# Kernel optimization log

Measured on AMD Instinct MI355X. Metric: run time of the kernel, lower is better.

The kernel has to match this reference:

```python
import jax, jax.numpy as jnp
import numpy as np

B, S, D, H, E, K, V, FF, P = 1, 2048, 1024, 16, 8, 2, 32000, 4096, 4096
HD = D // H
EPS = 1e-5


def setup_inputs() -> dict:
    key = jax.random.key(0)
    ks = iter(jax.random.split(key, 64))
    w = lambda shape: jax.random.normal(next(ks), shape, jnp.float32) * 0.02
    d = {}
    d['input_ids'] = jax.random.randint(next(ks), (B, S), 0, V)
    d['embed_w'] = w((V, D))
    d['pos_w'] = w((P, D))
    for i in (0, 1):
        d[f'b{i}_ln1_g'] = jnp.ones(D); d[f'b{i}_ln1_b'] = jnp.zeros(D)
        d[f'b{i}_in_w'] = w((3 * D, D)); d[f'b{i}_in_b'] = jnp.zeros(3 * D)
        d[f'b{i}_out_w'] = w((D, D)); d[f'b{i}_out_b'] = jnp.zeros(D)
        d[f'b{i}_ln2_g'] = jnp.ones(D); d[f'b{i}_ln2_b'] = jnp.zeros(D)
    d['b0_ffn_w1'] = w((FF, D)); d['b0_ffn_b1'] = jnp.zeros(FF)
    d['b0_ffn_w2'] = w((D, FF)); d['b0_ffn_b2'] = jnp.zeros(D)
    d['b1_gate_w'] = w((E, D)); d['b1_gate_b'] = jnp.zeros(E)
    d['b1_moe_w1'] = w((E, FF, D)); d['b1_moe_b1'] = jnp.zeros((E, FF))
    d['b1_moe_w2'] = w((E, D, FF)); d['b1_moe_b2'] = jnp.zeros((E, D))
    d['norm_g'] = jnp.ones(D); d['norm_b'] = jnp.zeros(D)
    d['head_w'] = w((V, D))
    return d


def _ln(x, g, b):
    m = jnp.mean(x, -1, keepdims=True)
    v = jnp.mean(jnp.square(x - m), -1, keepdims=True)
    return (x - m) * jax.lax.rsqrt(v + EPS) * g + b


def _mha(x, in_w, in_b, out_w, out_b):
    # torch nn.MultiheadAttention (batch_first, eval mode -> no dropout)
    qkv = x @ in_w.T + in_b  # [B,S,3D]
    q, k, v = jnp.split(qkv, 3, axis=-1)
    q = q.reshape(B, S, H, HD); k = k.reshape(B, S, H, HD); v = v.reshape(B, S, H, HD)
    scores = jnp.einsum('bqhd,bkhd->bhqk', q, k) / jnp.sqrt(jnp.float32(HD))
    attn = jax.nn.softmax(scores, axis=-1)
    o = jnp.einsum('bhqk,bkhd->bqhd', attn, v).reshape(B, S, D)
    return o @ out_w.T + out_b


def _moe(h, gate_w, gate_b, w1, b1, w2, b2):
    scores = h @ gate_w.T + gate_b                       # [B,S,E]
    top_s, top_i = jax.lax.top_k(scores, K)              # [B,S,K]
    weights = jax.nn.softmax(top_s, axis=-1)             # softmax over top-k
    onehot = jax.nn.one_hot(top_i, E, dtype=h.dtype)     # [B,S,K,E]
    combine = jnp.sum(onehot * weights[..., None], axis=-2)  # [B,S,E]
    hid = jax.nn.gelu(jnp.einsum('bsd,efd->bsef', h, w1) + b1, approximate=False)
    eo = jnp.einsum('bsef,edf->bsed', hid, w2) + b2      # [B,S,E,D]
    return jnp.einsum('bsed,bse->bsd', eo, combine)


def reference(input_ids, embed_w, pos_w,
              b0_ln1_g, b0_ln1_b, b0_in_w, b0_in_b, b0_out_w, b0_out_b, b0_ln2_g, b0_ln2_b,
              b0_ffn_w1, b0_ffn_b1, b0_ffn_w2, b0_ffn_b2,
              b1_ln1_g, b1_ln1_b, b1_in_w, b1_in_b, b1_out_w, b1_out_b, b1_ln2_g, b1_ln2_b,
              b1_gate_w, b1_gate_b, b1_moe_w1, b1_moe_b1, b1_moe_w2, b1_moe_b2,
              norm_g, norm_b, head_w):
    pos = jnp.arange(S)[None, :]
    x = jnp.take(embed_w, input_ids, axis=0) + jnp.take(pos_w, pos, axis=0)
    # block 0: dense FFN
    x = x + _mha(_ln(x, b0_ln1_g, b0_ln1_b), b0_in_w, b0_in_b, b0_out_w, b0_out_b)
    h = _ln(x, b0_ln2_g, b0_ln2_b)
    ffn = jax.nn.gelu(h @ b0_ffn_w1.T + b0_ffn_b1, approximate=False) @ b0_ffn_w2.T + b0_ffn_b2
    x = x + ffn  # integration layer assumed residual add
    # block 1: MoE
    x = x + _mha(_ln(x, b1_ln1_g, b1_ln1_b), b1_in_w, b1_in_b, b1_out_w, b1_out_b)
    h = _ln(x, b1_ln2_g, b1_ln2_b)
    x = x + _moe(h, b1_gate_w, b1_gate_b, b1_moe_w1, b1_moe_b1, b1_moe_w2, b1_moe_b2)
    x = _ln(x, norm_g, norm_b)
    return x @ head_w.T
```

## Files before the change

kernel.cpp:

```cpp
#include <hip/hip_runtime.h>
#include <hip/hip_bf16.h>
#include <math.h>

typedef unsigned short ushort_t;
typedef __attribute__((ext_vector_type(8))) __bf16 bf16x8;
typedef __attribute__((ext_vector_type(4))) float f32x4;
typedef __attribute__((ext_vector_type(8))) short s8v;
typedef __attribute__((ext_vector_type(4))) short s4v;

#define SQ 2048
#define DM 1024
#define NH 16
#define HDIM 64
#define FFD 4096
#define NVOC 32000

__device__ inline float b2f(unsigned short u) {
  union { unsigned int i; float f; } x; x.i = ((unsigned int)u) << 16; return x.f;
}
__device__ inline unsigned short f2b(float f) {
  __hip_bfloat16 h = __float2bfloat16(f);
  return *reinterpret_cast<unsigned short*>(&h);
}
__device__ inline void split2(float x, ushort_t& h, ushort_t& l) {
  h = f2b(x);
  l = f2b(x - b2f(h));
}
__device__ inline float geluf(float v) {
  return 0.5f * v * (1.0f + erff(v * 0.70710678118654752f));
}
__device__ __forceinline__ void gld16(const void* g, void* l) {
  __builtin_amdgcn_global_load_lds(
      (const __attribute__((address_space(1))) void*)g,
      (__attribute__((address_space(3))) void*)l, 16, 0, 0);
}
#define MFMA __builtin_amdgcn_mfma_f32_16x16x32_bf16

template<int EPI, int NT, int KS>
__device__ __forceinline__ void gemmsp_body(
    const ushort_t* __restrict__ AH, const ushort_t* __restrict__ AL,
    int lda, long long bA,
    const ushort_t* __restrict__ BH, const ushort_t* __restrict__ BL,
    int ldb, long long bB,
    float* __restrict__ C, ushort_t* __restrict__ CH, ushort_t* __restrict__ CL,
    int ldc, long long bC, long long pC,
    int M, int N, int K, const float* __restrict__ bias, float alpha,
    ushort_t* __restrict__ TH, ushort_t* __restrict__ TL)
{
  int z = blockIdx.z, h = z / KS, kc = z % KS;
  const ushort_t* AHp = AH + (long long)h * bA + (long long)kc * K;
  const ushort_t* ALp = AL + (long long)h * bA + (long long)kc * K;
  const ushort_t* BHp = BH + (long long)h * bB + (long long)kc * K;
  const ushort_t* BLp = BL + (long long)h * bB + (long long)kc * K;
  int m0 = blockIdx.x * 128, n0 = blockIdx.y * NT;
  const int NF = NT / 32;

  __shared__ __align__(16) ushort_t sAH[2][128 * 32], sAL[2][128 * 32];
  __shared__ __align__(16) ushort_t sBH[2][NT * 32],  sBL[2][NT * 32];

  int tid = threadIdx.x, lane = tid & 63, wave = tid >> 6;
  int wr = (wave >> 1) * 64, wc = (wave & 1) * (NT >> 1);
  int l15 = lane & 15, l4 = lane >> 4;

  f32x4 acc[4][NF];
#pragma unroll
  for (int m = 0; m < 4; ++m)
#pragma unroll
    for (int n = 0; n < NF; ++n) acc[m][n] = (f32x4){0.f, 0.f, 0.f, 0.f};

  auto stageG = [&](int buf, int k0) {
#pragma unroll
    for (int i = 0; i < 2; ++i) {
      int fi = i * 2048 + tid * 8;
      int r = fi >> 5, chk = (fi >> 3) & 3;
      int scol = ((chk ^ ((r >> 1) & 3)) << 3);
      int ra = m0 + r; if (ra > M - 1) ra = M - 1;
      long long go = (long long)ra * lda + k0 + scol;
      gld16(AHp + go, &sAH[buf][fi]);
      gld16(ALp + go, &sAL[buf][fi]);
    }
#pragma unroll
    for (int i = 0; i < NT / 64; ++i) {
      int fi = i * 2048 + tid * 8;
      int r = fi >> 5, chk = (fi >> 3) & 3;
      int scol = ((chk ^ ((r >> 1) & 3)) << 3);
      int rb = n0 + r; if (rb > N - 1) rb = N - 1;
      long long go = (long long)rb * ldb + k0 + scol;
      gld16(BHp + go, &sBH[buf][fi]);
      gld16(BLp + go, &sBL[buf][fi]);
    }
  };

  int nIt = K >> 5;
  stageG(0, 0);
  for (int it = 0; it < nIt; ++it) {
    int cur = it & 1;
    __syncthreads();
    if (it + 1 < nIt) stageG(cur ^ 1, (it + 1) << 5);
    bf16x8 ah[4], al[4], bh[NF], bl[NF];
#pragma unroll
    for (int m = 0; m < 4; ++m) {
      int r = wr + m * 16 + l15;
      int o = r * 32 + ((l4 ^ ((r >> 1) & 3)) << 3);
      ah[m] = *(const bf16x8*)&sAH[cur][o];
      al[m] = *(const bf16x8*)&sAL[cur][o];
    }
#pragma unroll
    for (int n = 0; n < NF; ++n) {
      int r = wc + n * 16 + l15;
      int o = r * 32 + ((l4 ^ ((r >> 1) & 3)) << 3);
      bh[n] = *(const bf16x8*)&sBH[cur][o];
      bl[n] = *(const bf16x8*)&sBL[cur][o];
    }
#pragma unroll
    for (int m = 0; m < 4; ++m)
#pragma unroll
      for (int n = 0; n < NF; ++n) {
        acc[m][n] = MFMA(ah[m], bh[n], acc[m][n], 0, 0, 0);
        acc[m][n] = MFMA(al[m], bh[n], acc[m][n], 0, 0, 0);
        acc[m][n] = MFMA(ah[m], bl[n], acc[m][n], 0, 0, 0);
      }
  }

  if (EPI == 5 && n0 >= 2 * DM) {
#pragma unroll
    for (int m = 0; m < 4; ++m) {
      int rbase = m0 + wr + m * 16 + l4 * 4;
#pragma unroll
      for (int n = 0; n < NF; ++n) {
        int c = n0 + wc + n * 16 + l15;
        int d = c - 2 * DM;
        float bv = bias[c];
        s4v hv, lv;
#pragma unroll
        for (int q = 0; q < 4; ++q) {
          ushort_t hh, ll; split2(acc[m][n][q] + bv, hh, ll);
          hv[q] = (short)hh; lv[q] = (short)ll;
        }
        *(s4v*)&TH[(long long)d * SQ + rbase] = hv;
        *(s4v*)&TL[(long long)d * SQ + rbase] = lv;
      }
    }
    return;
  }

#pragma unroll
  for (int m = 0; m < 4; ++m) {
#pragma unroll
    for (int n = 0; n < NF; ++n) {
      int c = n0 + wc + n * 16 + l15;
      if (c >= N) continue;
      float bv = (EPI == 4 || EPI == 5) ? bias[c] : 0.f;
#pragma unroll
      for (int q = 0; q < 4; ++q) {
        int rr = m0 + wr + m * 16 + l4 * 4 + q;
        if (rr >= M) continue;
        float v = acc[m][n][q];
        if (EPI == 5) {
          ushort_t hh, ll; split2(v + bv, hh, ll);
          long long o = (long long)rr * ldc + c; CH[o] = hh; CL[o] = ll;
        } else if (EPI == 2) {
          C[(long long)kc * pC + (long long)rr * ldc + (long long)h * bC + c] = v;
        } else if (EPI == 4) {
          ushort_t hh, ll; split2(geluf(v + bv), hh, ll);
          long long o = (long long)rr * ldc + c; CH[o] = hh; CL[o] = ll;
        }
      }
    }
  }
}

#define SP_ARGS const ushort_t* AH, const ushort_t* AL, int lda, long long bA, \
    const ushort_t* BH, const ushort_t* BL, int ldb, long long bB, \
    float* C, ushort_t* CH, ushort_t* CL, int ldc, long long bC, long long pC, \
    int M, int N, int K, const float* bias, float alpha, \
    ushort_t* TH, ushort_t* TL
#define SP_PASS AH, AL, lda, bA, BH, BL, ldb, bB, C, CH, CL, ldc, bC, pC, M, N, K, bias, alpha, TH, TL

__global__ __launch_bounds__(256) void k_qkv (SP_ARGS) { gemmsp_body<5,128,1>(SP_PASS); }
__global__ __launch_bounds__(256) void k_outp(SP_ARGS) { gemmsp_body<2, 64,4>(SP_PASS); }
__global__ __launch_bounds__(256) void k_ffn1(SP_ARGS) { gemmsp_body<4,128,1>(SP_PASS); }
__global__ __launch_bounds__(256) void k_ffn2(SP_ARGS) { gemmsp_body<2, 64,2>(SP_PASS); }

__global__ __launch_bounds__(256)
void k_attn(const ushort_t* __restrict__ qkvH, const ushort_t* __restrict__ qkvL,
            const ushort_t* __restrict__ VtH, const ushort_t* __restrict__ VtL,
            ushort_t* __restrict__ aH, ushort_t* __restrict__ aL)
{
  int f = blockIdx.x + blockIdx.y * gridDim.x;
  int logical = (f & 7) * 64 + (f >> 3);
  int q0 = (logical & 31) * 64;
  int h  = logical >> 5;

  __shared__ __align__(16) ushort_t sKH[2][4096], sKL[2][4096];
  __shared__ __align__(16) ushort_t sVH[2][4096], sVL[2][4096];
  __shared__ __align__(16) ushort_t sPH[4096], sPL[4096];

  int tid = threadIdx.x, lane = tid & 63, wave = tid >> 6;
  int l15 = lane & 15, l4 = lane >> 4;

  bf16x8 qh[2], ql[2];
  {
    long long base = (long long)(q0 + wave * 16 + l15) * (3 * DM) + h * 64 + l4 * 8;
    qh[0] = *(const bf16x8*)(qkvH + base);
    qh[1] = *(const bf16x8*)(qkvH + base + 32);
    ql[0] = *(const bf16x8*)(qkvL + base);
    ql[1] = *(const bf16x8*)(qkvL + base + 32);
  }

  auto stageKV = [&](int buf, int kt) {
#pragma unroll
    for (int i = 0; i < 2; ++i) {
      int idx = i * 2048 + tid * 8;
      int row = idx >> 6, chk = (idx >> 3) & 7;
      int scol = ((chk ^ (row & 7)) << 3);
      long long gk = (long long)(kt * 64 + row) * (3 * DM) + DM + h * 64 + scol;
      long long gv = (long long)(h * 64 + row) * SQ + kt * 64 + scol;
      gld16(qkvH + gk, &sKH[buf][idx]);
      gld16(qkvL + gk, &sKL[buf][idx]);
      gld16(VtH + gv, &sVH[buf][idx]);
      gld16(VtL + gv, &sVL[buf][idx]);
    }
  };

  float mrow[4], lrow[4];
  f32x4 Oacc[4];
#pragma unroll
  for (int r = 0; r < 4; ++r) { mrow[r] = -1e30f; lrow[r] = 0.f; }
#pragma unroll
  for (int n = 0; n < 4; ++n) Oacc[n] = (f32x4){0.f, 0.f, 0.f, 0.f};

  const int NT = SQ / 64;
  stageKV(0, 0);
  for (int kt = 0; kt < NT; ++kt) {
    int cur = kt & 1;
    __syncthreads();
    if (kt + 1 < NT) stageKV(cur ^ 1, kt + 1);

    f32x4 S[4];
#pragma unroll
    for (int n = 0; n < 4; ++n) S[n] = (f32x4){0.f, 0.f, 0.f, 0.f};
#pragma unroll
    for (int kk = 0; kk < 64; kk += 32) {
      int kkI = kk >> 5;
      bf16x8 qhf = qh[kkI], qlf = ql[kkI];
#pragma unroll
      for (int n = 0; n < 4; ++n) {
        int br = n * 16 + l15;
        int bo = br * 64 + ((((kk >> 3) + l4) ^ (br & 7)) << 3);
        bf16x8 kh = *(const bf16x8*)&sKH[cur][bo];
        bf16x8 kl = *(const bf16x8*)&sKL[cur][bo];
        S[n] = MFMA(qhf, kh, S[n], 0, 0, 0);
        S[n] = MFMA(qlf, kh, S[n], 0, 0, 0);
        S[n] = MFMA(qhf, kl, S[n], 0, 0, 0);
      }
    }
    float tm[4], ts[4];
#pragma unroll
    for (int r = 0; r < 4; ++r) {
#pragma unroll
      for (int n = 0; n < 4; ++n) S[n][r] *= 0.125f;
      tm[r] = fmaxf(fmaxf(S[0][r], S[1][r]), fmaxf(S[2][r], S[3][r]));
    }
#pragma unroll
    for (int mk = 1; mk <= 8; mk <<= 1)
#pragma unroll
      for (int r = 0; r < 4; ++r) tm[r] = fmaxf(tm[r], __shfl_xor(tm[r], mk));
#pragma unroll
    for (int r = 0; r < 4; ++r) {
      float mn = fmaxf(mrow[r], tm[r]);
      float corr = __expf(mrow[r] - mn);
      mrow[r] = mn;
      float s = 0.f;
#pragma unroll
      for (int n = 0; n < 4; ++n) { S[n][r] = __expf(S[n][r] - mn); s += S[n][r]; }
      ts[r] = s;
      lrow[r] *= corr;
#pragma unroll
      for (int n = 0; n < 4; ++n) Oacc[n][r] *= corr;
    }
#pragma unroll
    for (int mk = 1; mk <= 8; mk <<= 1)
#pragma unroll
      for (int r = 0; r < 4; ++r) ts[r] += __shfl_xor(ts[r], mk);
#pragma unroll
    for (int r = 0; r < 4; ++r) lrow[r] += ts[r];

    {
      ushort_t* pH = &sPH[wave * 1024];
      ushort_t* pL = &sPL[wave * 1024];
#pragma unroll
      for (int n = 0; n < 4; ++n)
#pragma unroll
        for (int r = 0; r < 4; ++r) {
          int row = l4 * 4 + r, col = n * 16 + l15;
          int ad = row * 64 + (((col >> 3) ^ (row & 7)) << 3) + (col & 7);
          ushort_t hh, ll; split2(S[n][r], hh, ll);
          pH[ad] = hh; pL[ad] = ll;
        }
    }
    __syncthreads();
#pragma unroll
    for (int kk = 0; kk < 64; kk += 32) {
      int ao = wave * 1024 + l15 * 64 + ((((kk >> 3) + l4) ^ (l15 & 7)) << 3);
      bf16x8 ph = *(const bf16x8*)&sPH[ao];
      bf16x8 pl = *(const bf16x8*)&sPL[ao];
#pragma unroll
      for (int n = 0; n < 4; ++n) {
        int br = n * 16 + l15;
        int bo = br * 64 + ((((kk >> 3) + l4) ^ (br & 7)) << 3);
        bf16x8 vh = *(const bf16x8*)&sVH[cur][bo];
        bf16x8 vl = *(const bf16x8*)&sVL[cur][bo];
        Oacc[n] = MFMA(ph, vh, Oacc[n], 0, 0, 0);
        Oacc[n] = MFMA(pl, vh, Oacc[n], 0, 0, 0);
        Oacc[n] = MFMA(ph, vl, Oacc[n], 0, 0, 0);
      }
    }
  }

#pragma unroll
  for (int n = 0; n < 4; ++n)
#pragma unroll
    for (int r = 0; r < 4; ++r) {
      int q = q0 + wave * 16 + l4 * 4 + r;
      int d = h * 64 + n * 16 + l15;
      float val = Oacc[n][r] / lrow[r];
      ushort_t hh, ll; split2(val, hh, ll);
      long long o = (long long)q * DM + d;
      aH[o] = hh; aL[o] = ll;
    }
}

template<int EPI, int SWAP, int KS>
__device__ __forceinline__ void gemm16s_body(
    const ushort_t* __restrict__ A, int lda, long long bA,
    const ushort_t* __restrict__ Bp0, int ldb, long long bB,
    void* __restrict__ Cv, int ldc, long long bC, long long pC,
    int M, int N, int K, const float* __restrict__ bias, int bBias,
    const int* __restrict__ offs)
{
  int bz = blockIdx.z;
  int z = bz / KS, kc = bz % KS;
  int Kc = K / KS;
  const ushort_t* Ap = A + (long long)z * bA + (long long)kc * Kc;
  const ushort_t* Bp = Bp0 + (long long)z * bB + (long long)kc * Kc;
  int rowStart = 0, Meff = M;
  if (offs) { rowStart = offs[z]; Meff = offs[z + 1] - rowStart; }
  int m0 = (SWAP ? blockIdx.y : blockIdx.x) * 128;
  if (m0 >= Meff) return;
  int n0 = (SWAP ? blockIdx.x : blockIdx.y) * 128;

  __shared__ __align__(16) char smem[32768];

  int tid = threadIdx.x, lane = tid & 63, wave = tid >> 6;
  int wr = (wave >> 1) * 64, wc = (wave & 1) * 64;
  int l15 = lane & 15, l4 = lane >> 4;

  f32x4 acc[4][4];
#pragma unroll
  for (int m = 0; m < 4; ++m)
#pragma unroll
    for (int n = 0; n < 4; ++n) acc[m][n] = (f32x4){0.f, 0.f, 0.f, 0.f};

  auto stageG = [&](int buf, int k0) {
    ushort_t* dA = (ushort_t*)(smem + buf * 8192);
    ushort_t* dB = (ushort_t*)(smem + 16384 + buf * 8192);
#pragma unroll
    for (int i = 0; i < 2; ++i) {
      int idx = i * 2048 + tid * 8;
      int row = idx >> 5, chk = (idx >> 3) & 3;
      int scol = ((chk ^ ((row >> 1) & 3)) << 3);
      int ra = m0 + row; if (ra > Meff - 1) ra = Meff - 1;
      gld16(Ap + (long long)(rowStart + ra) * lda + k0 + scol, &dA[idx]);
    }
#pragma unroll
    for (int i = 0; i < 2; ++i) {
      int idx = i * 2048 + tid * 8;
      int row = idx >> 5, chk = (idx >> 3) & 3;
      int scol = ((chk ^ ((row >> 1) & 3)) << 3);
      int rb = n0 + row; if (rb > N - 1) rb = N - 1;
      gld16(Bp + (long long)rb * ldb + k0 + scol, &dB[idx]);
    }
  };

  int nIt = Kc >> 5;
  stageG(0, 0);
  for (int it = 0; it < nIt; ++it) {
    int cur = it & 1;
    __syncthreads();
    if (it + 1 < nIt) stageG(cur ^ 1, (it + 1) << 5);
    ushort_t* As = (ushort_t*)(smem + cur * 8192);
    ushort_t* Bs = (ushort_t*)(smem + 16384 + cur * 8192);
    bf16x8 af[4], bfr[4];
#pragma unroll
    for (int m = 0; m < 4; ++m) {
      int r = wr + m * 16 + l15;
      af[m] = *(const bf16x8*)&As[r * 32 + ((l4 ^ ((r >> 1) & 3)) << 3)];
    }
#pragma unroll
    for (int n = 0; n < 4; ++n) {
      int r = wc + n * 16 + l15;
      bfr[n] = *(const bf16x8*)&Bs[r * 32 + ((l4 ^ ((r >> 1) & 3)) << 3)];
    }
#pragma unroll
    for (int m = 0; m < 4; ++m)
#pragma unroll
      for (int n = 0; n < 4; ++n)
        acc[m][n] = MFMA(af[m], bfr[n], acc[m][n], 0, 0, 0);
  }
  __syncthreads();

  if (EPI == 7) {
    float* fE = (float*)smem;
#pragma unroll
    for (int h2 = 0; h2 < 2; ++h2) {
      if ((wave >> 1) == h2) {
#pragma unroll
        for (int m = 0; m < 4; ++m)
#pragma unroll
          for (int n = 0; n < 4; ++n)
#pragma unroll
            for (int q = 0; q < 4; ++q)
              fE[(m * 16 + l4 * 4 + q) * 128 + wc + n * 16 + l15] = acc[m][n][q];
      }
      __syncthreads();
#pragma unroll
      for (int i = 0; i < 8; ++i) {
        int lin = tid + i * 256;
        int row = lin >> 5, c4 = (lin & 31) << 2;
        int gr = m0 + h2 * 64 + row;
        if (gr < Meff) {
          f32x4 v4 = *(const f32x4*)&fE[row * 128 + c4];
          long long crow = rowStart + gr;
          float* dst = (float*)Cv + (long long)kc * pC + crow * ldc + n0 + c4;
          *(f32x4*)dst = v4;
        }
      }
      __syncthreads();
    }
    return;
  }

#pragma unroll
  for (int m = 0; m < 4; ++m) {
#pragma unroll
    for (int n = 0; n < 4; ++n) {
      int c = n0 + wc + n * 16 + l15;
      if (c >= N) continue;
      float bv = (EPI == 2) ? bias[(long long)z * bBias + c] : 0.f;
#pragma unroll
      for (int q = 0; q < 4; ++q) {
        int rr = m0 + wr + m * 16 + l4 * 4 + q;
        if (rr >= Meff) continue;
        float v = acc[m][n][q];
        long long crow = rowStart + rr;
        if (EPI == 2)
          ((ushort_t*)Cv)[crow * ldc + (long long)z * bC + c] = f2b(geluf(v + bv));
      }
    }
  }
}

template<int BSRC>
__device__ __forceinline__ void gemm16w_body(
    const ushort_t* __restrict__ A, int lda,
    const void* __restrict__ Bv, int ldb,
    float* __restrict__ Cv, int ldc,
    int M, int N, int K)
{
  int bx = blockIdx.x, by = blockIdx.y;
  {
    int flat = bx + by * gridDim.x;
    int cpx = (gridDim.x * gridDim.y) >> 3;
    int s = (flat & 7) * cpx + (flat >> 3);
    bx = s % gridDim.x; by = s / gridDim.x;
  }
  int m0 = bx * 256;
  int n0 = by * 128;

  __shared__ __align__(16) char smem[49152];
  const ushort_t* Bp = (BSRC == 1) ? (const ushort_t*)Bv : nullptr;
  const float* Bf = (BSRC == 0) ? (const float*)Bv : nullptr;

  int tid = threadIdx.x, lane = tid & 63, wave = tid >> 6;
  int wr = (wave >> 1) * 128, wc = (wave & 1) * 64;
  int l15 = lane & 15, l4 = lane >> 4;

  f32x4 acc[8][4];
#pragma unroll
  for (int m = 0; m < 8; ++m)
#pragma unroll
    for (int n = 0; n < 4; ++n) acc[m][n] = (f32x4){0.f, 0.f, 0.f, 0.f};

  auto stageG = [&](int buf, int k0) {
    ushort_t* dA = (ushort_t*)(smem + buf * 16384);
    ushort_t* dB = (ushort_t*)(smem + 32768 + buf * 8192);
#pragma unroll
    for (int i = 0; i < 4; ++i) {
      int idx = i * 2048 + tid * 8;
      int row = idx >> 5, chk = (idx >> 3) & 3;
      int scol = ((chk ^ ((row >> 1) & 3)) << 3);
      int ra = m0 + row; if (ra > M - 1) ra = M - 1;
      gld16(A + (long long)ra * lda + k0 + scol, &dA[idx]);
    }
    if (BSRC == 1) {
#pragma unroll
      for (int i = 0; i < 2; ++i) {
        int idx = i * 2048 + tid * 8;
        int row = idx >> 5, chk = (idx >> 3) & 3;
        int scol = ((chk ^ ((row >> 1) & 3)) << 3);
        int rb = n0 + row; if (rb > N - 1) rb = N - 1;
        gld16(Bp + (long long)rb * ldb + k0 + scol, &dB[idx]);
      }
    } else {
#pragma unroll
      for (int i = 0; i < 4; ++i) {
        int g = tid + i * 256;
        int r = g >> 3, c4 = (g & 7) * 4;
        int rb = n0 + r; if (rb > N - 1) rb = N - 1;
        float4 fv = *(const float4*)(Bf + (long long)rb * ldb + k0 + c4);
        s4v o; o[0] = (short)f2b(fv.x); o[1] = (short)f2b(fv.y);
        o[2] = (short)f2b(fv.z); o[3] = (short)f2b(fv.w);
        int dst = r * 32 + ((((c4 >> 3) ^ ((r >> 1) & 3))) << 3) + (c4 & 7);
        *(s4v*)&dB[dst] = o;
      }
    }
  };

  int nIt = K >> 5;
  stageG(0, 0);
  for (int it = 0; it < nIt; ++it) {
    int cur = it & 1;
    __syncthreads();
    if (it + 1 < nIt) stageG(cur ^ 1, (it + 1) << 5);
    ushort_t* As = (ushort_t*)(smem + cur * 16384);
    ushort_t* Bs = (ushort_t*)(smem + 32768 + cur * 8192);
    bf16x8 af[8], bfr[4];
#pragma unroll
    for (int m = 0; m < 8; ++m) {
      int r = wr + m * 16 + l15;
      af[m] = *(const bf16x8*)&As[r * 32 + ((l4 ^ ((r >> 1) & 3)) << 3)];
    }
#pragma unroll
    for (int n = 0; n < 4; ++n) {
      int r = wc + n * 16 + l15;
      bfr[n] = *(const bf16x8*)&Bs[r * 32 + ((l4 ^ ((r >> 1) & 3)) << 3)];
    }
#pragma unroll
    for (int m = 0; m < 8; ++m)
#pragma unroll
      for (int n = 0; n < 4; ++n)
        acc[m][n] = MFMA(af[m], bfr[n], acc[m][n], 0, 0, 0);
  }
  __syncthreads();

  float* fE = (float*)smem;
#pragma unroll
  for (int h2 = 0; h2 < 4; ++h2) {
    if ((wave >> 1) == (h2 >> 1)) {
#pragma unroll
      for (int mm = 0; mm < 4; ++mm) {
        int m = (h2 & 1) * 4 + mm;
#pragma unroll
        for (int n = 0; n < 4; ++n)
#pragma unroll
          for (int q = 0; q < 4; ++q)
            fE[(mm * 16 + l4 * 4 + q) * 128 + wc + n * 16 + l15] = acc[m][n][q];
      }
    }
    __syncthreads();
#pragma unroll
    for (int i = 0; i < 8; ++i) {
      int lin = tid + i * 256;
      int row = lin >> 5, c4 = (lin & 31) << 2;
      int gr = m0 + h2 * 64 + row;
      if (gr < M) {
        f32x4 v4 = *(const f32x4*)&fE[row * 128 + c4];
        float* dst = Cv + (long long)gr * ldc + n0 + c4;
        __builtin_nontemporal_store(v4, (f32x4*)dst);
      }
    }
    __syncthreads();
  }
}

#define G16_ARGS const ushort_t* A, int lda, long long bA, const void* Bv, \
    int ldb, long long bB, void* Cv, int ldc, long long bC, long long pC, \
    int M, int N, int K, const float* bias, int bBias, const int* offs
#define G16S_PASS(EPI,SWAP,KS) gemm16s_body<EPI,SWAP,KS>(A, lda, bA, \
    (const ushort_t*)Bv, ldb, bB, Cv, ldc, bC, pC, M, N, K, bias, bBias, offs)

__global__ __launch_bounds__(256) void k_moe1(G16_ARGS) { G16S_PASS(2,1,1); }
__global__ __launch_bounds__(256) void k_moe2(G16_ARGS) { G16S_PASS(7,1,2); }
__global__ __launch_bounds__(256) void k_head_bf(G16_ARGS) {
  gemm16w_body<1>(A, lda, Bv, ldb, (float*)Cv, ldc, M, N, K);
}
__global__ __launch_bounds__(256) void k_head_f(G16_ARGS) {
  gemm16w_body<0>(A, lda, Bv, ldb, (float*)Cv, ldc, M, N, K);
}

__global__ __launch_bounds__(256)
void cvt_split2(const float* __restrict__ s0, ushort_t* __restrict__ dh0,
                ushort_t* __restrict__ dl0,
                const float* __restrict__ s1, ushort_t* __restrict__ dh1,
                ushort_t* __restrict__ dl1, int n4)
{
  const float* s = blockIdx.y ? s1 : s0;
  ushort_t* dh = blockIdx.y ? dh1 : dh0;
  ushort_t* dl = blockIdx.y ? dl1 : dl0;
  int i = blockIdx.x * blockDim.x + threadIdx.x;
  int stride = gridDim.x * blockDim.x;
  for (; i < n4; i += stride) {
    float4 f = ((const float4*)s)[i];
    s4v h, l; ushort_t hh, ll;
    split2(f.x, hh, ll); h[0] = (short)hh; l[0] = (short)ll;
    split2(f.y, hh, ll); h[1] = (short)hh; l[1] = (short)ll;
    split2(f.z, hh, ll); h[2] = (short)hh; l[2] = (short)ll;
    split2(f.w, hh, ll); h[3] = (short)hh; l[3] = (short)ll;
    ((s4v*)dh)[i] = h; ((s4v*)dl)[i] = l;
  }
}

__global__ __launch_bounds__(256)
void cvt_bf16(const float* __restrict__ s, ushort_t* __restrict__ d, int n4)
{
  int i = blockIdx.x * blockDim.x + threadIdx.x;
  int stride = gridDim.x * blockDim.x;
  for (; i < n4; i += stride) {
    float4 f = ((const float4*)s)[i];
    s4v o; o[0] = (short)f2b(f.x); o[1] = (short)f2b(f.y);
    o[2] = (short)f2b(f.z); o[3] = (short)f2b(f.w);
    ((s4v*)d)[i] = o;
  }
}

__global__ __launch_bounds__(256)
void cvt_bf16_2(const float* __restrict__ s0, ushort_t* __restrict__ d0,
                const float* __restrict__ s1, ushort_t* __restrict__ d1, int n4)
{
  const float* s = blockIdx.y ? s1 : s0;
  ushort_t* d = blockIdx.y ? d1 : d0;
  int i = blockIdx.x * blockDim.x + threadIdx.x;
  int stride = gridDim.x * blockDim.x;
  for (; i < n4; i += stride) {
    float4 f = ((const float4*)s)[i];
    s4v o; o[0] = (short)f2b(f.x); o[1] = (short)f2b(f.y);
    o[2] = (short)f2b(f.z); o[3] = (short)f2b(f.w);
    ((s4v*)d)[i] = o;
  }
}

__global__ __launch_bounds__(256)
void embed_kernel(const int* __restrict__ ids, const float* __restrict__ ew,
                  const float* __restrict__ pw, float* __restrict__ x,
                  int* __restrict__ counts)
{
  int srow = blockIdx.x, tid = threadIdx.x;
  if (srow == 0 && tid < 8) counts[tid] = 0;
  int id = ids[srow];
  const float4 e = *(const float4*)(ew + (long long)id * DM + tid * 4);
  const float4 p = *(const float4*)(pw + (long long)srow * DM + tid * 4);
  float4* xr = (float4*)(x + (long long)srow * DM) + tid;
  *xr = make_float4(e.x + p.x, e.y + p.y, e.z + p.z, e.w + p.w);
}

template<int MODE, int NP>
__global__ __launch_bounds__(256)
void ln_fused(float* __restrict__ x, const float* __restrict__ P, long long pC,
              const float* __restrict__ bias_pre,
              const float* __restrict__ g, const float* __restrict__ b,
              ushort_t* __restrict__ outH, ushort_t* __restrict__ outL)
{
  int row = blockIdx.x, tid = threadIdx.x;
  long long xo = (long long)row * DM + tid * 4;
  float4 v = *(const float4*)(x + xo);
  if (NP > 0) {
    float4 bp = *(const float4*)(bias_pre + tid * 4);
    float sx = bp.x, sy = bp.y, sz = bp.z, sw = bp.w;
#pragma unroll
    for (int p = 0; p < NP; ++p) {
      float4 pv = *(const float4*)(P + (long long)p * pC + xo);
      sx += pv.x; sy += pv.y; sz += pv.z; sw += pv.w;
    }
    v.x += sx; v.y += sy; v.z += sz; v.w += sw;
    *(float4*)(x + xo) = v;
  }
  __shared__ float sm1[4], sm2[4];
  float s = v.x + v.y + v.z + v.w;
  for (int o = 32; o > 0; o >>= 1) s += __shfl_down(s, o);
  if ((tid & 63) == 0) sm1[tid >> 6] = s;
  __syncthreads();
  float mean = (sm1[0] + sm1[1] + sm1[2] + sm1[3]) * (1.0f / DM);
  float d0 = v.x - mean, d1 = v.y - mean, d2 = v.z - mean, d3 = v.w - mean;
  float q = d0 * d0 + d1 * d1 + d2 * d2 + d3 * d3;
  for (int o = 32; o > 0; o >>= 1) q += __shfl_down(q, o);
  if ((tid & 63) == 0) sm2[tid >> 6] = q;
  __syncthreads();
  float var = (sm2[0] + sm2[1] + sm2[2] + sm2[3]) * (1.0f / DM);
  float rstd = rsqrtf(var + 1e-5f);
  float4 gv = ((const float4*)g)[tid];
  float4 bv = ((const float4*)b)[tid];
  float o0 = d0 * rstd * gv.x + bv.x, o1 = d1 * rstd * gv.y + bv.y;
  float o2 = d2 * rstd * gv.z + bv.z, o3 = d3 * rstd * gv.w + bv.w;
  long long base = (long long)row * DM + tid * 4;
  if (MODE == 0) {
    ushort_t hh, ll;
    split2(o0, hh, ll); outH[base + 0] = hh; outL[base + 0] = ll;
    split2(o1, hh, ll); outH[base + 1] = hh; outL[base + 1] = ll;
    split2(o2, hh, ll); outH[base + 2] = hh; outL[base + 2] = ll;
    split2(o3, hh, ll); outH[base + 3] = hh; outL[base + 3] = ll;
  } else {
    outH[base + 0] = f2b(o0); outH[base + 1] = f2b(o1);
    outH[base + 2] = f2b(o2); outH[base + 3] = f2b(o3);
  }
}

__global__ __launch_bounds__(256)
void ln_gate_top2(float* __restrict__ x, const float* __restrict__ P,
                  long long pC, const float* __restrict__ bias_pre,
                  const float* __restrict__ g, const float* __restrict__ b,
                  const float* __restrict__ gw, const float* __restrict__ gb,
                  int* __restrict__ topi, float* __restrict__ topw,
                  int* __restrict__ counts, ushort_t* __restrict__ outH)
{
  int row = blockIdx.x, tid = threadIdx.x;
  long long xo = (long long)row * DM + tid * 4;
  float4 v = *(const float4*)(x + xo);
  {
    float4 bp = *(const float4*)(bias_pre + tid * 4);
    float sx = bp.x, sy = bp.y, sz = bp.z, sw = bp.w;
#pragma unroll
    for (int p = 0; p < 4; ++p) {
      float4 pv = *(const float4*)(P + (long long)p * pC + xo);
      sx += pv.x; sy += pv.y; sz += pv.z; sw += pv.w;
    }
    v.x += sx; v.y += sy; v.z += sz; v.w += sw;
    *(float4*)(x + xo) = v;
  }
  __shared__ float sm1[4], sm2[4];
  __shared__ float se[8][4];
  float s = v.x + v.y + v.z + v.w;
  for (int o = 32; o > 0; o >>= 1) s += __shfl_down(s, o);
  if ((tid & 63) == 0) sm1[tid >> 6] = s;
  __syncthreads();
  float mean = (sm1[0] + sm1[1] + sm1[2] + sm1[3]) * (1.0f / DM);
  float d0 = v.x - mean, d1 = v.y - mean, d2 = v.z - mean, d3 = v.w - mean;
  float q = d0 * d0 + d1 * d1 + d2 * d2 + d3 * d3;
  for (int o = 32; o > 0; o >>= 1) q += __shfl_down(q, o);
  if ((tid & 63) == 0) sm2[tid >> 6] = q;
  __syncthreads();
  float var = (sm2[0] + sm2[1] + sm2[2] + sm2[3]) * (1.0f / DM);
  float rstd = rsqrtf(var + 1e-5f);
  float4 gv = ((const float4*)g)[tid];
  float4 bv = ((const float4*)b)[tid];
  float h0 = d0 * rstd * gv.x + bv.x, h1 = d1 * rstd * gv.y + bv.y;
  float h2 = d2 * rstd * gv.z + bv.z, h3 = d3 * rstd * gv.w + bv.w;
  long long base = (long long)row * DM + tid * 4;
  outH[base + 0] = f2b(h0); outH[base + 1] = f2b(h1);
  outH[base + 2] = f2b(h2); outH[base + 3] = f2b(h3);
#pragma unroll
  for (int e = 0; e < 8; ++e) {
    float4 w = ((const float4*)(gw + (long long)e * DM))[tid];
    float p = h0 * w.x + h1 * w.y + h2 * w.z + h3 * w.w;
    for (int o = 32; o > 0; o >>= 1) p += __shfl_down(p, o);
    if ((tid & 63) == 0) se[e][tid >> 6] = p;
  }
  __syncthreads();
  if (tid == 0) {
    float sc[8];
#pragma unroll
    for (int e = 0; e < 8; ++e)
      sc[e] = se[e][0] + se[e][1] + se[e][2] + se[e][3] + gb[e];
    int i1 = 0; float m1 = sc[0];
    for (int e = 1; e < 8; ++e) if (sc[e] > m1) { m1 = sc[e]; i1 = e; }
    int i2 = -1; float m2 = -1e30f;
    for (int e = 0; e < 8; ++e) if (e != i1 && sc[e] > m2) { m2 = sc[e]; i2 = e; }
    float e2 = __expf(m2 - m1);
    float w1 = 1.f / (1.f + e2);
    topi[row * 2] = i1; topi[row * 2 + 1] = i2;
    topw[row * 2] = w1; topw[row * 2 + 1] = 1.f - w1;
    atomicAdd(&counts[i1], 1);
    atomicAdd(&counts[i2], 1);
  }
}

__global__ void moe_prefix(const int* __restrict__ counts, int* __restrict__ offs,
                           int* __restrict__ cursors)
{
  if (threadIdx.x == 0 && blockIdx.x == 0) {
    int a = 0;
    for (int e = 0; e < 8; ++e) { offs[e] = a; a += counts[e]; cursors[e] = 0; }
    offs[8] = a;
  }
}

__global__ __launch_bounds__(256)
void moe_gather(const ushort_t* __restrict__ hH, const int* __restrict__ topi,
                const float* __restrict__ topw, const int* __restrict__ offs,
                int* __restrict__ cursors, int* __restrict__ tokIdx,
                float* __restrict__ tokW, int* __restrict__ slotOf,
                ushort_t* __restrict__ Xg)
{
  int tok = blockIdx.x, tid = threadIdx.x;
  __shared__ int s0s, s1s;
  if (tid == 0) {
    int e0 = topi[tok * 2], e1 = topi[tok * 2 + 1];
    int s0 = offs[e0] + atomicAdd(&cursors[e0], 1);
    int s1 = offs[e1] + atomicAdd(&cursors[e1], 1);
    tokIdx[s0] = tok; tokW[s0] = topw[tok * 2];
    tokIdx[s1] = tok; tokW[s1] = topw[tok * 2 + 1];
    slotOf[tok * 2] = s0; slotOf[tok * 2 + 1] = s1;
    s0s = s0; s1s = s1;
  }
  __syncthreads();
  s4v v = ((const s4v*)(hH + (long long)tok * DM))[tid];
  ((s4v*)(Xg + (long long)s0s * DM))[tid] = v;
  ((s4v*)(Xg + (long long)s1s * DM))[tid] = v;
}

__global__ __launch_bounds__(256)
void moe_ln_final(const float* __restrict__ x, const float* __restrict__ eo,
                  long long pC, const int* __restrict__ slotOf,
                  const int* __restrict__ topi, const float* __restrict__ topw,
                  const float* __restrict__ b2, const float* __restrict__ g,
                  const float* __restrict__ b, ushort_t* __restrict__ outH)
{
  int tok = blockIdx.x, tid = threadIdx.x;
  int s0 = slotOf[tok * 2], s1 = slotOf[tok * 2 + 1];
  int e0 = topi[tok * 2], e1 = topi[tok * 2 + 1];
  float w0 = topw[tok * 2], w1 = topw[tok * 2 + 1];
  float4 a  = ((const float4*)(eo + (long long)s0 * DM))[tid];
  float4 a2 = ((const float4*)(eo + pC + (long long)s0 * DM))[tid];
  float4 bb1= ((const float4*)(eo + (long long)s1 * DM))[tid];
  float4 bb2= ((const float4*)(eo + pC + (long long)s1 * DM))[tid];
  float4 ba = ((const float4*)(b2 + (long long)e0 * DM))[tid];
  float4 bbb= ((const float4*)(b2 + (long long)e1 * DM))[tid];
  float4 v = ((const float4*)(x + (long long)tok * DM))[tid];
  v.x += w0 * (a.x + a2.x + ba.x) + w1 * (bb1.x + bb2.x + bbb.x);
  v.y += w0 * (a.y + a2.y + ba.y) + w1 * (bb1.y + bb2.y + bbb.y);
  v.z += w0 * (a.z + a2.z + ba.z) + w1 * (bb1.z + bb2.z + bbb.z);
  v.w += w0 * (a.w + a2.w + ba.w) + w1 * (bb1.w + bb2.w + bbb.w);
  __shared__ float sm1[4], sm2[4];
  float s = v.x + v.y + v.z + v.w;
  for (int o = 32; o > 0; o >>= 1) s += __shfl_down(s, o);
  if ((tid & 63) == 0) sm1[tid >> 6] = s;
  __syncthreads();
  float mean = (sm1[0] + sm1[1] + sm1[2] + sm1[3]) * (1.0f / DM);
  float d0 = v.x - mean, d1 = v.y - mean, d2 = v.z - mean, d3 = v.w - mean;
  float q = d0 * d0 + d1 * d1 + d2 * d2 + d3 * d3;
  for (int o = 32; o > 0; o >>= 1) q += __shfl_down(q, o);
  if ((tid & 63) == 0) sm2[tid >> 6] = q;
  __syncthreads();
  float var = (sm2[0] + sm2[1] + sm2[2] + sm2[3]) * (1.0f / DM);
  float rstd = rsqrtf(var + 1e-5f);
  float4 gv = ((const float4*)g)[tid];
  float4 bv = ((const float4*)b)[tid];
  long long base = (long long)tok * DM + tid * 4;
  outH[base + 0] = f2b(d0 * rstd * gv.x + bv.x);
  outH[base + 1] = f2b(d1 * rstd * gv.y + bv.y);
  outH[base + 2] = f2b(d2 * rstd * gv.z + bv.z);
  outH[base + 3] = f2b(d3 * rstd * gv.w + bv.w);
}

extern "C" void kernel_launch(void* const* d_in, const int* in_sizes, int n_in,
                              void* d_out, int out_size, void* d_ws, size_t ws_size,
                              hipStream_t stream)
{
  const int* ids = (const int*)d_in[0];
  const float* embed_w = (const float*)d_in[1];
  const float* pos_w   = (const float*)d_in[2];
  const float* ln1_g[2] = {(const float*)d_in[3],  (const float*)d_in[11]};
  const float* ln1_b[2] = {(const float*)d_in[4],  (const float*)d_in[12]};
  const float* in_w[2]  = {(const float*)d_in[5],  (const float*)d_in[13]};
  const float* in_b[2]  = {(const float*)d_in[6],  (const float*)d_in[14]};
  const float* out_w[2] = {(const float*)d_in[7],  (const float*)d_in[15]};
  const float* out_b[2] = {(const float*)d_in[8],  (const float*)d_in[16]};
  const float* ln2_g[2] = {(const float*)d_in[9],  (const float*)d_in[17]};
  const float* ln2_b[2] = {(const float*)d_in[10], (const float*)d_in[18]};
  const float* ffn_w1 = (const float*)d_in[19];
  const float* ffn_b1 = (const float*)d_in[20];
  const float* ffn_w2 = (const float*)d_in[21];
  const float* ffn_b2 = (const float*)d_in[22];
  const float* gate_w = (const float*)d_in[23];
  const float* gate_b = (const float*)d_in[24];
  const float* moe_w1 = (const float*)d_in[25];
  const float* moe_b1 = (const float*)d_in[26];
  const float* moe_w2 = (const float*)d_in[27];
  const float* moe_b2 = (const float*)d_in[28];
  const float* norm_g = (const float*)d_in[29];
  const float* norm_b = (const float*)d_in[30];
  const float* head_w = (const float*)d_in[31];

  char* ob = (char*)d_out;
  size_t off = 0;
  auto alloc = [&](size_t bytes) {
    char* p = ob + off;
    off = (off + bytes + 255) & ~(size_t)255;
    return p;
  };
  float*    x      = (float*)alloc((size_t)SQ * DM * 4);
  ushort_t* hbufH  = (ushort_t*)alloc((size_t)SQ * DM * 2);
  ushort_t* hbufL  = (ushort_t*)alloc((size_t)SQ * DM * 2);
  ushort_t* qkvH   = (ushort_t*)alloc((size_t)SQ * 3 * DM * 2);
  ushort_t* qkvL   = (ushort_t*)alloc((size_t)SQ * 3 * DM * 2);
  ushort_t* VtH    = (ushort_t*)alloc((size_t)NH * HDIM * SQ * 2);
  ushort_t* VtL    = (ushort_t*)alloc((size_t)NH * HDIM * SQ * 2);
  char*     resv   = (char*)alloc((size_t)32 << 20);
  ushort_t* attnH  = (ushort_t*)alloc((size_t)SQ * DM * 2);
  ushort_t* attnL  = (ushort_t*)alloc((size_t)SQ * DM * 2);
  ushort_t* Xg     = (ushort_t*)alloc((size_t)2 * SQ * DM * 2);
  int*      topi   = (int*)alloc(SQ * 2 * 4);
  float*    topw   = (float*)alloc(SQ * 2 * 4);
  int*      tokIdx = (int*)alloc(2 * SQ * 4);
  float*    tokW   = (float*)alloc(2 * SQ * 4);
  int*      slotOf = (int*)alloc(2 * SQ * 4);
  int*      counts = (int*)alloc(256);
  int*      offsb  = (int*)alloc(256);
  int*      cursors= (int*)alloc(256);
  ushort_t* ffnH   = (ushort_t*)alloc((size_t)SQ * FFD * 2);
  ushort_t* ffnL   = (ushort_t*)alloc((size_t)SQ * FFD * 2);
  float*    eo     = (float*)alloc((size_t)2 * 2 * SQ * DM * 4);
  ushort_t* inwH[2], *inwL[2], *outwH[2], *outwL[2];
  ushort_t* wsplit0 = (ushort_t*)alloc(0);
  inwH[0]  = (ushort_t*)alloc((size_t)3 * DM * DM * 2);
  inwL[0]  = (ushort_t*)alloc((size_t)3 * DM * DM * 2);
  inwH[1]  = (ushort_t*)alloc((size_t)3 * DM * DM * 2);
  inwL[1]  = (ushort_t*)alloc((size_t)3 * DM * DM * 2);
  outwH[0] = (ushort_t*)alloc((size_t)DM * DM * 2);
  outwL[0] = (ushort_t*)alloc((size_t)DM * DM * 2);
  outwH[1] = (ushort_t*)alloc((size_t)DM * DM * 2);
  outwL[1] = (ushort_t*)alloc((size_t)DM * DM * 2);
  ushort_t* f1H = (ushort_t*)alloc((size_t)FFD * DM * 2);
  ushort_t* f1L = (ushort_t*)alloc((size_t)FFD * DM * 2);
  ushort_t* f2H = (ushort_t*)alloc((size_t)DM * FFD * 2);
  ushort_t* f2L = (ushort_t*)alloc((size_t)DM * FFD * 2);
  ushort_t* moe_w1b = wsplit0;
  ushort_t* moe_w2b = qkvH;
  ushort_t* moehid  = ffnH;
  float*    pp      = eo;
  const long long eoPC = (long long)2 * SQ * DM;
  const long long ppPC = (long long)SQ * DM;
  ushort_t* hfin    = (ushort_t*)d_ws;
  bool wsBig = ws_size >= ((size_t)70 << 20);
  ushort_t* head_wb = (ushort_t*)((char*)d_ws + ((size_t)4 << 20));
  (void)resv;

  embed_kernel<<<SQ, 256, 0, stream>>>(ids, embed_w, pos_w, x, counts);
  cvt_split2<<<dim3(512, 2), 256, 0, stream>>>(
      in_w[0], inwH[0], inwL[0], in_w[1], inwH[1], inwL[1], 3 * DM * DM / 4);
  cvt_split2<<<dim3(512, 2), 256, 0, stream>>>(
      out_w[0], outwH[0], outwL[0], out_w[1], outwH[1], outwL[1], DM * DM / 4);
  cvt_split2<<<dim3(512, 2), 256, 0, stream>>>(
      ffn_w1, f1H, f1L, ffn_w2, f2H, f2L, FFD * DM / 4);
  if (wsBig)
    cvt_bf16<<<1024, 256, 0, stream>>>(head_w, head_wb, NVOC * DM / 4);

  ln_fused<0, 0><<<SQ, 256, 0, stream>>>(x, nullptr, 0, nullptr,
                                         ln1_g[0], ln1_b[0], hbufH, hbufL);
  k_qkv<<<dim3(16, 24, 1), 256, 0, stream>>>(
      hbufH, hbufL, DM, 0, inwH[0], inwL[0], DM, 0,
      nullptr, qkvH, qkvL, 3 * DM, 0, 0,
      SQ, 3 * DM, DM, in_b[0], 1.f, VtH, VtL);
  k_attn<<<dim3(SQ / 64, NH), 256, 0, stream>>>(qkvH, qkvL, VtH, VtL,
                                                attnH, attnL);
  k_outp<<<dim3(16, 16, 4), 256, 0, stream>>>(
      attnH, attnL, DM, 0, outwH[0], outwL[0], DM, 0,
      pp, nullptr, nullptr, DM, 0, ppPC,
      SQ, DM, DM / 4, nullptr, 1.f, nullptr, nullptr);
  ln_fused<0, 4><<<SQ, 256, 0, stream>>>(x, pp, ppPC, out_b[0],
                                         ln2_g[0], ln2_b[0], hbufH, hbufL);
  k_ffn1<<<dim3(16, 32, 1), 256, 0, stream>>>(
      hbufH, hbufL, DM, 0, f1H, f1L, DM, 0,
      nullptr, ffnH, ffnL, FFD, 0, 0,
      SQ, FFD, DM, ffn_b1, 1.f, nullptr, nullptr);
  k_ffn2<<<dim3(16, 16, 2), 256, 0, stream>>>(
      ffnH, ffnL, FFD, 0, f2H, f2L, FFD, 0,
      pp, nullptr, nullptr, DM, 0, ppPC,
      SQ, DM, FFD / 2, nullptr, 1.f, nullptr, nullptr);
  ln_fused<0, 2><<<SQ, 256, 0, stream>>>(x, pp, ppPC, ffn_b2,
                                         ln1_g[1], ln1_b[1], hbufH, hbufL);
  k_qkv<<<dim3(16, 24, 1), 256, 0, stream>>>(
      hbufH, hbufL, DM, 0, inwH[1], inwL[1], DM, 0,
      nullptr, qkvH, qkvL, 3 * DM, 0, 0,
      SQ, 3 * DM, DM, in_b[1], 1.f, VtH, VtL);
  k_attn<<<dim3(SQ / 64, NH), 256, 0, stream>>>(qkvH, qkvL, VtH, VtL,
                                                attnH, attnL);
  k_outp<<<dim3(16, 16, 4), 256, 0, stream>>>(
      attnH, attnL, DM, 0, outwH[1], outwL[1], DM, 0,
      pp, nullptr, nullptr, DM, 0, ppPC,
      SQ, DM, DM / 4, nullptr, 1.f, nullptr, nullptr);
  cvt_bf16_2<<<dim3(2048, 2), 256, 0, stream>>>(
      moe_w1, moe_w1b, moe_w2, moe_w2b, 8 * FFD * DM / 4);
  ln_gate_top2<<<SQ, 256, 0, stream>>>(x, pp, ppPC, out_b[1],
                                       ln2_g[1], ln2_b[1], gate_w, gate_b,
                                       topi, topw, counts, hbufH);
  moe_prefix<<<1, 64, 0, stream>>>(counts, offsb, cursors);
  moe_gather<<<SQ, 256, 0, stream>>>(hbufH, topi, topw, offsb, cursors,
                                     tokIdx, tokW, slotOf, Xg);
  k_moe1<<<dim3(32, 16, 8), 256, 0, stream>>>(
      Xg, DM, 0, moe_w1b, DM, (long long)FFD * DM,
      moehid, FFD, 0, 0, SQ, FFD, DM, moe_b1, FFD, offsb);
  k_moe2<<<dim3(8, 16, 16), 256, 0, stream>>>(
      moehid, FFD, 0, moe_w2b, FFD, (long long)DM * FFD,
      eo, DM, 0, eoPC, SQ, DM, FFD, nullptr, 0, offsb);
  moe_ln_final<<<SQ, 256, 0, stream>>>(x, eo, eoPC, slotOf, topi, topw,
                                       moe_b2, norm_g, norm_b, hfin);
  if (wsBig)
    k_head_bf<<<dim3(8, 250, 1), 256, 0, stream>>>(
        hfin, DM, 0, head_wb, DM, 0, d_out, NVOC, 0, 0,
        SQ, NVOC, DM, nullptr, 0, nullptr);
  else
    k_head_f<<<dim3(8, 250, 1), 256, 0, stream>>>(
        hfin, DM, 0, head_w, DM, 0, d_out, NVOC, 0, 0,
        SQ, NVOC, DM, nullptr, 0, nullptr);
}
```

Measured before the change: 1.126 ms.

## Deepen bf16 head GEMM prefetch to two stages with explicit vmcnt waits

The bf16-weight vocab-head GEMM now gets its own body. It issues global-to-LDS loads two k-steps ahead and uses manual s_waitcnt vmcnt counts plus raw s_barrier in place of __syncthreads each iteration. LDS fragments are read into registers before the barrier, so the next stage can overwrite the same buffer while the MFMAs run. The fp32-weight path is split into a separate unchanged function. The aim is to hide global load latency in the large head GEMM, at the cost of fragile hand-tuned wait counts.

```diff
diff --git a/kernel.cpp b/kernel.cpp
--- a/kernel.cpp
+++ b/kernel.cpp
@@ -461,10 +461,9 @@
   }
 }
 
-template<int BSRC>
-__device__ __forceinline__ void gemm16w_body(
+__device__ __forceinline__ void gemm16w8_body(
     const ushort_t* __restrict__ A, int lda,
-    const void* __restrict__ Bv, int ldb,
+    const ushort_t* __restrict__ Bp, int ldb,
     float* __restrict__ Cv, int ldc,
     int M, int N, int K)
 {
@@ -479,8 +478,6 @@
   int n0 = by * 128;
 
   __shared__ __align__(16) char smem[49152];
-  const ushort_t* Bp = (BSRC == 1) ? (const ushort_t*)Bv : nullptr;
-  const float* Bf = (BSRC == 0) ? (const float*)Bv : nullptr;
 
   int tid = threadIdx.x, lane = tid & 63, wave = tid >> 6;
   int wr = (wave >> 1) * 128, wc = (wave & 1) * 64;
@@ -503,27 +500,138 @@
       int ra = m0 + row; if (ra > M - 1) ra = M - 1;
       gld16(A + (long long)ra * lda + k0 + scol, &dA[idx]);
     }
-    if (BSRC == 1) {
-#pragma unroll
-      for (int i = 0; i < 2; ++i) {
-        int idx = i * 2048 + tid * 8;
-        int row = idx >> 5, chk = (idx >> 3) & 3;
-        int scol = ((chk ^ ((row >> 1) & 3)) << 3);
-        int rb = n0 + row; if (rb > N - 1) rb = N - 1;
-        gld16(Bp + (long long)rb * ldb + k0 + scol, &dB[idx]);
+#pragma unroll
+    for (int i = 0; i < 2; ++i) {
+      int idx = i * 2048 + tid * 8;
+      int row = idx >> 5, chk = (idx >> 3) & 3;
+      int scol = ((chk ^ ((row >> 1) & 3)) << 3);
+      int rb = n0 + row; if (rb > N - 1) rb = N - 1;
+      gld16(Bp + (long long)rb * ldb + k0 + scol, &dB[idx]);
+    }
+  };
+
+  int nIt = K >> 5;
+  stageG(0, 0);
+  stageG(1, 32);
+  asm volatile("s_waitcnt vmcnt(6)" ::: "memory");
+  __builtin_amdgcn_s_barrier();
+  __builtin_amdgcn_sched_barrier(0);
+
+  for (int it = 0; it < nIt; ++it) {
+    int cur = it & 1;
+    ushort_t* As = (ushort_t*)(smem + cur * 16384);
+    ushort_t* Bs = (ushort_t*)(smem + 32768 + cur * 8192);
+    bf16x8 af[8], bfr[4];
+#pragma unroll
+    for (int m = 0; m < 8; ++m) {
+      int r = wr + m * 16 + l15;
+      af[m] = *(const bf16x8*)&As[r * 32 + ((l4 ^ ((r >> 1) & 3)) << 3)];
+    }
+#pragma unroll
+    for (int n = 0; n < 4; ++n) {
+      int r = wc + n * 16 + l15;
+      bfr[n] = *(const bf16x8*)&Bs[r * 32 + ((l4 ^ ((r >> 1) & 3)) << 3)];
+    }
+    asm volatile("s_waitcnt lgkmcnt(0)" ::: "memory");
+    __builtin_amdgcn_sched_barrier(0);
+    __builtin_amdgcn_s_barrier();
+    __builtin_amdgcn_sched_barrier(0);
+    if (it + 2 < nIt) stageG(cur, (it + 2) << 5);
+#pragma unroll
+    for (int m = 0; m < 8; ++m)
+#pragma unroll
+      for (int n = 0; n < 4; ++n)
+        acc[m][n] = MFMA(af[m], bfr[n], acc[m][n], 0, 0, 0);
+    if (it + 1 < nIt) {
+      if (it + 2 < nIt)
+        asm volatile("s_waitcnt vmcnt(6)" ::: "memory");
+      else
+        asm volatile("s_waitcnt vmcnt(0)" ::: "memory");
+      __builtin_amdgcn_s_barrier();
+      __builtin_amdgcn_sched_barrier(0);
+    }
+  }
+  __syncthreads();
+
+  float* fE = (float*)smem;
+#pragma unroll
+  for (int h2 = 0; h2 < 4; ++h2) {
+    if ((wave >> 1) == (h2 >> 1)) {
+#pragma unroll
+      for (int mm = 0; mm < 4; ++mm) {
+        int m = (h2 & 1) * 4 + mm;
+#pragma unroll
+        for (int n = 0; n < 4; ++n)
+#pragma unroll
+          for (int q = 0; q < 4; ++q)
+            fE[(mm * 16 + l4 * 4 + q) * 128 + wc + n * 16 + l15] = acc[m][n][q];
       }
-    } else {
-#pragma unroll
-      for (int i = 0; i < 4; ++i) {
-        int g = tid + i * 256;
-        int r = g >> 3, c4 = (g & 7) * 4;
-        int rb = n0 + r; if (rb > N - 1) rb = N - 1;
-        float4 fv = *(const float4*)(Bf + (long long)rb * ldb + k0 + c4);
-        s4v o; o[0] = (short)f2b(fv.x); o[1] = (short)f2b(fv.y);
-        o[2] = (short)f2b(fv.z); o[3] = (short)f2b(fv.w);
-        int dst = r * 32 + ((((c4 >> 3) ^ ((r >> 1) & 3))) << 3) + (c4 & 7);
-        *(s4v*)&dB[dst] = o;
+    }
+    __syncthreads();
+#pragma unroll
+    for (int i = 0; i < 8; ++i) {
+      int lin = tid + i * 256;
+      int row = lin >> 5, c4 = (lin & 31) << 2;
+      int gr = m0 + h2 * 64 + row;
+      if (gr < M) {
+        f32x4 v4 = *(const f32x4*)&fE[row * 128 + c4];
+        float* dst = Cv + (long long)gr * ldc + n0 + c4;
+        __builtin_nontemporal_store(v4, (f32x4*)dst);
       }
+    }
+    __syncthreads();
+  }
+}
+
+__device__ __forceinline__ void gemm16w_body_f(
+    const ushort_t* __restrict__ A, int lda,
+    const float* __restrict__ Bf, int ldb,
+    float* __restrict__ Cv, int ldc,
+    int M, int N, int K)
+{
+  int bx = blockIdx.x, by = blockIdx.y;
+  {
+    int flat = bx + by * gridDim.x;
+    int cpx = (gridDim.x * gridDim.y) >> 3;
+    int s = (flat & 7) * cpx + (flat >> 3);
+    bx = s % gridDim.x; by = s / gridDim.x;
+  }
+  int m0 = bx * 256;
+  int n0 = by * 128;
+
+  __shared__ __align__(16) char smem[49152];
+
+  int tid = threadIdx.x, lane = tid & 63, wave = tid >> 6;
+  int wr = (wave >> 1) * 128, wc = (wave & 1) * 64;
+  int l15 = lane & 15, l4 = lane >> 4;
+
+  f32x4 acc[8][4];
+#pragma unroll
+  for (int m = 0; m < 8; ++m)
+#pragma unroll
+    for (int n = 0; n < 4; ++n) acc[m][n] = (f32x4){0.f, 0.f, 0.f, 0.f};
+
+  auto stageG = [&](int buf, int k0) {
+    ushort_t* dA = (ushort_t*)(smem + buf * 16384);
+    ushort_t* dB = (ushort_t*)(smem + 32768 + buf * 8192);
+#pragma unroll
+    for (int i = 0; i < 4; ++i) {
+      int idx = i * 2048 + tid * 8;
+      int row = idx >> 5, chk = (idx >> 3) & 3;
+      int scol = ((chk ^ ((row >> 1) & 3)) << 3);
+      int ra = m0 + row; if (ra > M - 1) ra = M - 1;
+      gld16(A + (long long)ra * lda + k0 + scol, &dA[idx]);
+    }
+#pragma unroll
+    for (int i = 0; i < 4; ++i) {
+      int g = tid + i * 256;
+      int r = g >> 3, c4 = (g & 7) * 4;
+      int rb = n0 + r; if (rb > N - 1) rb = N - 1;
+      float4 fv = *(const float4*)(Bf + (long long)rb * ldb + k0 + c4);
+      s4v o; o[0] = (short)f2b(fv.x); o[1] = (short)f2b(fv.y);
+      o[2] = (short)f2b(fv.z); o[3] = (short)f2b(fv.w);
+      int dst = r * 32 + ((((c4 >> 3) ^ ((r >> 1) & 3))) << 3) + (c4 & 7);
+      *(s4v*)&dB[dst] = o;
     }
   };
 
@@ -593,10 +701,10 @@
 __global__ __launch_bounds__(256) void k_moe1(G16_ARGS) { G16S_PASS(2,1,1); }
 __global__ __launch_bounds__(256) void k_moe2(G16_ARGS) { G16S_PASS(7,1,2); }
 __global__ __launch_bounds__(256) void k_head_bf(G16_ARGS) {
-  gemm16w_body<1>(A, lda, Bv, ldb, (float*)Cv, ldc, M, N, K);
+  gemm16w8_body(A, lda, (const ushort_t*)Bv, ldb, (float*)Cv, ldc, M, N, K);
 }
 __global__ __launch_bounds__(256) void k_head_f(G16_ARGS) {
-  gemm16w_body<0>(A, lda, Bv, ldb, (float*)Cv, ldc, M, N, K);
+  gemm16w_body_f(A, lda, (const float*)Bv, ldb, (float*)Cv, ldc, M, N, K);
 }
 
 __global__ __launch_bounds__(256)
```

Result: no change. 1.131 ms (+0.5%).
